# Kernel tuning notes

Measured on AMD Instinct MI355X. Metric: run time of the kernel, lower is better.

Reference implementation:

```python
import jax, jax.numpy as jnp
import numpy as np

DIM = 512
HIDDEN = int(DIM * 0.2)  # 102
K_TOKENS = 64
N_TOKENS = 65536
LN_EPS = 1e-5


def setup_inputs() -> dict:
    key = jax.random.key(0)
    ks = jax.random.split(key, 8)
    x = jax.random.normal(ks[0], (N_TOKENS, DIM), dtype=jnp.float32)
    ln_gamma = jnp.ones((DIM,), dtype=jnp.float32)
    ln_beta = jnp.zeros((DIM,), dtype=jnp.float32)
    W1 = jax.random.normal(ks[1], (DIM, HIDDEN), dtype=jnp.float32) / np.sqrt(DIM)
    b1 = jnp.zeros((HIDDEN,), dtype=jnp.float32)
    W2 = jax.random.normal(ks[2], (HIDDEN, K_TOKENS), dtype=jnp.float32) / np.sqrt(HIDDEN)
    b2 = jnp.zeros((K_TOKENS,), dtype=jnp.float32)
    scale = jnp.ones((1, 1), dtype=jnp.float32)
    return {
        "x": x,
        "ln_gamma": ln_gamma,
        "ln_beta": ln_beta,
        "W1": W1,
        "b1": b1,
        "W2": W2,
        "b2": b2,
        "scale": scale,
        "keeped_tokens": K_TOKENS,
    }


def reference(x, ln_gamma, ln_beta, W1, b1, W2, b2, scale, keeped_tokens):
    # LayerNorm over last dim
    mu = jnp.mean(x, axis=-1, keepdims=True)
    var = jnp.mean(jnp.square(x - mu), axis=-1, keepdims=True)
    h = (x - mu) * jax.lax.rsqrt(var + LN_EPS) * ln_gamma + ln_beta
    # fc1 + exact GELU (torch default) + dynamic fc2 scorer
    h = jax.nn.gelu(h @ W1 + b1, approximate=False)  # [N, HIDDEN]
    w = h @ W2 + b2                                   # [N, K]
    # transpose, scale, softmax over tokens
    w = w.T * scale                                   # [K, N]
    w = jax.nn.softmax(w, axis=1)
    # weighted token aggregation
    return w @ x                                      # [K, DIM]
```

## Files before the change

### kernel.cpp

```cpp
#include <hip/hip_runtime.h>
#include <math.h>

#define N_TOK 65536
#define DIM   512
#define HID   102
#define KTOK  64
#define NTILE 4096
#define LN_EPS 1e-5f

typedef __attribute__((ext_vector_type(8))) short short8;
typedef __attribute__((ext_vector_type(4))) float f32x4;

#define WS_LOGITS 0u
#define WS_PART   4194304u
#define WS_PM     (WS_PART + 4194304u)
#define WS_PS     (WS_PM + 262144u)
#define WS_W1F    (WS_PS + 262144u)
#define WS_W2F    (WS_W1F + 32768u)
#define WS_UB     (WS_W2F + 4096u)
#define WS_VV     (WS_UB + 128u)
#define WS_SMAX   (WS_VV + 128u)
#define WS_SINV   (WS_SMAX + 64u)

__device__ __forceinline__ unsigned short f2bf(float f) {
    unsigned int u = __float_as_uint(f);
    unsigned int r = (u + 0x7fffu + ((u >> 16) & 1u)) >> 16;
    return (unsigned short)r;
}
__device__ __forceinline__ float bf2f(unsigned short h) {
    return __uint_as_float(((unsigned int)h) << 16);
}

__device__ __forceinline__ void gload_lds16(const void* g, void* l) {
    __builtin_amdgcn_global_load_lds(
        (const __attribute__((address_space(1))) unsigned int*)g,
        (__attribute__((address_space(3))) unsigned int*)l, 16, 0, 0);
}

__device__ __forceinline__ void bar_lds() {
    asm volatile("s_waitcnt lgkmcnt(0)" ::: "memory");
    __builtin_amdgcn_s_barrier();
    __builtin_amdgcn_sched_barrier(0);
}

__global__ __launch_bounds__(256) void prep_k(const float* __restrict__ W1,
                                              const float* __restrict__ gamma,
                                              const float* __restrict__ W2,
                                              unsigned short* __restrict__ W1f,
                                              unsigned short* __restrict__ W2f) {
    const int idx = blockIdx.x * 256 + threadIdx.x;
    {
        const int e = idx & 7, lane = (idx >> 3) & 63;
        const int jj = (idx >> 9) & 7, kc = (idx >> 12) & 15;
        const int j = jj * 16 + (lane & 15);
        const int d = kc * 32 + (lane >> 4) * 8 + e;
        W1f[idx] = (j < HID) ? f2bf(gamma[d] * W1[d * HID + j]) : (unsigned short)0;
    }
    if (idx < 8192) {
        const int e = idx & 7, lane = (idx >> 3) & 63;
        const int kc = (idx >> 9) & 3, N = (idx >> 11) & 3;
        const int j = kc * 32 + (lane >> 4) * 8 + e;
        const int k = N * 16 + (lane & 15);
        W2f[idx] = (j < HID) ? f2bf(W2[j * KTOK + k]) : (unsigned short)0;
    }
}

__global__ __launch_bounds__(512) void prep2_k(const float* __restrict__ W1,
                                               const float* __restrict__ b1,
                                               const float* __restrict__ gamma,
                                               const float* __restrict__ beta,
                                               float* __restrict__ ub,
                                               float* __restrict__ vv) {
    __shared__ float su[4][128], sv[4][128];
    const int t = threadIdx.x;
    const int j = t & 127, q = t >> 7;
    float u = 0.0f, v = 0.0f;
    if (j < HID) {
        #pragma unroll 8
        for (int d = q * 128; d < q * 128 + 128; ++d) {
            const float wv = W1[d * HID + j];
            u = fmaf(beta[d], wv, u);
            v = fmaf(gamma[d], wv, v);
        }
    }
    su[q][j] = u; sv[q][j] = v;
    __syncthreads();
    if (q == 0) {
        ub[j] = su[0][j] + su[1][j] + su[2][j] + su[3][j] +
                ((j < HID) ? b1[j] : 0.0f);
        vv[j] = sv[0][j] + sv[1][j] + sv[2][j] + sv[3][j];
    }
}

__global__ __launch_bounds__(512) void scorer_k(const float* __restrict__ x,
                                                const unsigned short* __restrict__ W1f,
                                                const unsigned short* __restrict__ W2f,
                                                const float* __restrict__ ub,
                                                const float* __restrict__ vv,
                                                const float* __restrict__ b2,
                                                const float* __restrict__ scale,
                                                float* __restrict__ logits,
                                                float* __restrict__ pm,
                                                float* __restrict__ psum) {
    __shared__ char smem[4 * 8192];
    const int tid = threadIdx.x;
    const int lane = tid & 63;
    const int w = tid >> 6;
    const int l15 = lane & 15;
    const int hi = lane >> 4;
    const int tile = blockIdx.x * 8 + w;
    const int wt0 = tile * 16;
    char* hb = smem + w * 4096;

    const float* xrow = x + (size_t)(wt0 + l15) * DIM + hi * 8;

    f32x4 xva[5], xvb[5];
    xva[0] = *(const f32x4*)(xrow);
    xvb[0] = *(const f32x4*)(xrow + 4);
    xva[1] = *(const f32x4*)(xrow + 32);
    xvb[1] = *(const f32x4*)(xrow + 36);
    xva[2] = *(const f32x4*)(xrow + 64);
    xvb[2] = *(const f32x4*)(xrow + 68);
    gload_lds16(W1f + w * 512 + lane * 8, smem + w * 1024);
    xva[3] = *(const f32x4*)(xrow + 96);
    xvb[3] = *(const f32x4*)(xrow + 100);
    gload_lds16(W1f + 4096 + w * 512 + lane * 8, smem + 8192 + w * 1024);
    gload_lds16(W1f + 8192 + w * 512 + lane * 8, smem + 16384 + w * 1024);

    f32x4 acc[8] = {};
    float s = 0.0f, ss = 0.0f;
    #pragma unroll
    for (int kc = 0; kc < 16; ++kc) {
        if (kc < 12) {
            xva[(kc + 4) % 5] = *(const f32x4*)(xrow + (kc + 4) * 32);
            xvb[(kc + 4) % 5] = *(const f32x4*)(xrow + (kc + 4) * 32 + 4);
        }
        if (kc <= 1)       asm volatile("s_waitcnt vmcnt(6)" ::: "memory");
        else if (kc <= 11) asm volatile("s_waitcnt vmcnt(8)" ::: "memory");
        else if (kc == 12) asm volatile("s_waitcnt vmcnt(6)" ::: "memory");
        else if (kc == 13) asm volatile("s_waitcnt vmcnt(4)" ::: "memory");
        else if (kc == 14) asm volatile("s_waitcnt vmcnt(1)" ::: "memory");
        else               asm volatile("s_waitcnt vmcnt(0)" ::: "memory");
        __builtin_amdgcn_sched_barrier(0);
        __builtin_amdgcn_s_barrier();
        if (kc < 13) {
            gload_lds16(W1f + (kc + 3) * 4096 + w * 512 + lane * 8,
                        smem + ((kc + 3) & 3) * 8192 + w * 1024);
        }
        const f32x4 a = xva[kc % 5];
        const f32x4 b = xvb[kc % 5];
        s += a.x + a.y + a.z + a.w + b.x + b.y + b.z + b.w;
        ss += a.x * a.x + a.y * a.y + a.z * a.z + a.w * a.w +
              b.x * b.x + b.y * b.y + b.z * b.z + b.w * b.w;
        short8 af;
        af[0] = (short)f2bf(a.x); af[1] = (short)f2bf(a.y);
        af[2] = (short)f2bf(a.z); af[3] = (short)f2bf(a.w);
        af[4] = (short)f2bf(b.x); af[5] = (short)f2bf(b.y);
        af[6] = (short)f2bf(b.z); af[7] = (short)f2bf(b.w);
        const char* bb = smem + (kc & 3) * 8192 + lane * 16;
        __builtin_amdgcn_s_setprio(1);
        #pragma unroll
        for (int jj = 0; jj < 8; ++jj) {
            const short8 bf = *(const short8*)(bb + jj * 1024);
            acc[jj] = __builtin_amdgcn_mfma_f32_16x16x32_bf16(af, bf, acc[jj], 0, 0, 0);
        }
        __builtin_amdgcn_s_setprio(0);
    }
    __syncthreads();

    s += __shfl_xor(s, 16); ss += __shfl_xor(ss, 16);
    s += __shfl_xor(s, 32); ss += __shfl_xor(ss, 32);
    const float mu = s * (1.0f / 512.0f);
    const float inv = rsqrtf(ss * (1.0f / 512.0f) - mu * mu + LN_EPS);

    float invr[4], muir[4];
    #pragma unroll
    for (int r = 0; r < 4; ++r) {
        const int tk = 4 * hi + r;
        const float m_ = __shfl(mu, tk);
        const float i_ = __shfl(inv, tk);
        invr[r] = i_;
        muir[r] = m_ * i_;
    }
    #pragma unroll
    for (int jj = 0; jj < 8; ++jj) {
        const int col = jj * 16 + l15;
        const float ubj = ub[col];
        const float vvj = vv[col];
        #pragma unroll
        for (int reg = 0; reg < 4; ++reg) {
            const int t = 4 * hi + reg;
            const float pre = fmaf(invr[reg], acc[jj][reg],
                                   fmaf(-muir[reg], vvj, ubj));
            const float g = 0.5f * pre * (1.0f + erff(pre * 0.70710678118f));
            *(unsigned short*)(hb + t * 256 + ((col * 2) ^ ((t & 7) << 4))) = f2bf(g);
        }
    }
    asm volatile("s_waitcnt lgkmcnt(0)" ::: "memory");
    __builtin_amdgcn_sched_barrier(0);

    f32x4 acc2[4] = {};
    {
        const unsigned short* w2 = W2f + lane * 8;
        #pragma unroll
        for (int kc = 0; kc < 4; ++kc) {
            const short8 a2 = *(const short8*)(hb + l15 * 256 +
                                               ((kc * 64 + hi * 16) ^ ((l15 & 7) << 4)));
            __builtin_amdgcn_s_setprio(1);
            #pragma unroll
            for (int nt = 0; nt < 4; ++nt) {
                const short8 bfr = *(const short8*)(w2 + (size_t)(nt * 4 + kc) * 512);
                acc2[nt] = __builtin_amdgcn_mfma_f32_16x16x32_bf16(a2, bfr, acc2[nt], 0, 0, 0);
            }
            __builtin_amdgcn_s_setprio(0);
        }
    }

    const float sc = scale[0];
    #pragma unroll
    for (int nt = 0; nt < 4; ++nt) {
        const int k = nt * 16 + l15;
        const float bb = b2[k];
        f32x4 lv;
        lv.x = (acc2[nt][0] + bb) * sc;
        lv.y = (acc2[nt][1] + bb) * sc;
        lv.z = (acc2[nt][2] + bb) * sc;
        lv.w = (acc2[nt][3] + bb) * sc;
        *(f32x4*)(logits + (size_t)k * N_TOK + wt0 + hi * 4) = lv;
        float m4 = fmaxf(fmaxf(lv.x, lv.y), fmaxf(lv.z, lv.w));
        float s4 = __expf(lv.x - m4) + __expf(lv.y - m4) +
                   __expf(lv.z - m4) + __expf(lv.w - m4);
        #pragma unroll
        for (int o = 16; o <= 32; o <<= 1) {
            const float om = __shfl_xor(m4, o);
            const float os = __shfl_xor(s4, o);
            const float nm = fmaxf(m4, om);
            s4 = s4 * __expf(m4 - nm) + os * __expf(om - nm);
            m4 = nm;
        }
        if (hi == 0) {
            pm[tile * 64 + k] = m4;
            psum[tile * 64 + k] = s4;
        }
    }
}

__global__ __launch_bounds__(256) void stats_k(const float* __restrict__ pm,
                                               const float* __restrict__ psum,
                                               float* __restrict__ smax,
                                               float* __restrict__ sinv) {
    const int k = blockIdx.x;
    const int tid = threadIdx.x;
    __shared__ float rm[4], rs[4];
    float m = -1e30f, s = 0.0f;
    for (int b = tid; b < NTILE; b += 256) {
        const float pmv = pm[b * 64 + k];
        const float psv = psum[b * 64 + k];
        const float nm = fmaxf(m, pmv);
        s = s * __expf(m - nm) + psv * __expf(pmv - nm);
        m = nm;
    }
    #pragma unroll
    for (int o = 32; o >= 1; o >>= 1) {
        const float om = __shfl_xor(m, o);
        const float os = __shfl_xor(s, o);
        const float nm = fmaxf(m, om);
        s = s * __expf(m - nm) + os * __expf(om - nm);
        m = nm;
    }
    if ((tid & 63) == 0) { rm[tid >> 6] = m; rs[tid >> 6] = s; }
    __syncthreads();
    if (tid == 0) {
        float fm = rm[0], fs = rs[0];
        for (int i = 1; i < 4; ++i) {
            const float nm = fmaxf(fm, rm[i]);
            fs = fs * __expf(fm - nm) + rs[i] * __expf(rm[i] - nm);
            fm = nm;
        }
        smax[k] = fm;
        sinv[k] = 1.0f / fs;
    }
}

__global__ __launch_bounds__(512) void agg_k(const float* __restrict__ x,
                                             const float* __restrict__ logits,
                                             const float* __restrict__ smax,
                                             const float* __restrict__ sinv,
                                             float* __restrict__ part) {
    __shared__ char fsm[40960];
    const int tid = threadIdx.x;
    const int lane = tid & 63;
    const int w = tid >> 6;
    const int l15 = lane & 15;
    const int hi = lane >> 4;
    const int dg = blockIdx.y;
    const int tb = blockIdx.x;

    const int sk = tid >> 3;
    const int snp = (tid & 7) * 8;
    const int xd = tid & 127;
    const int xnb = (tid >> 7) * 16;
    const float mk = smax[sk];
    const float ik = sinv[sk];
    const float* lrow = logits + (size_t)sk * N_TOK + tb * 512 + snp;
    const float* xcol = x + (size_t)(tb * 512 + xnb) * DIM + dg * 128 + xd;

    char* pw = fsm + (((sk >> 4) * 2 + (snp >> 5)) * 64 +
                      (sk & 15) + 16 * ((snp & 31) >> 3)) * 16;
    const int xoff0 = (((xd >> 4) * 2 + (xnb >> 5)) * 64 +
                       (xd & 15) + 16 * (((xnb & 31) >> 3) + 0)) * 16;
    const int xoff1 = (((xd >> 4) * 2 + (xnb >> 5)) * 64 +
                       (xd & 15) + 16 * (((xnb & 31) >> 3) + 1)) * 16;

    const int kt = w & 3;
    const int dgr = w >> 2;

    f32x4 acc[4] = {};

    f32x4 pa = *(const f32x4*)(lrow);
    f32x4 pb = *(const f32x4*)(lrow + 4);
    float xl[16];
    #pragma unroll
    for (int i = 0; i < 16; ++i) xl[i] = xcol[(size_t)i * DIM];

    for (int c = 0; c < 8; ++c) {
        {
            short8 pv;
            pv[0] = (short)f2bf(__expf(pa.x - mk) * ik);
            pv[1] = (short)f2bf(__expf(pa.y - mk) * ik);
            pv[2] = (short)f2bf(__expf(pa.z - mk) * ik);
            pv[3] = (short)f2bf(__expf(pa.w - mk) * ik);
            pv[4] = (short)f2bf(__expf(pb.x - mk) * ik);
            pv[5] = (short)f2bf(__expf(pb.y - mk) * ik);
            pv[6] = (short)f2bf(__expf(pb.z - mk) * ik);
            pv[7] = (short)f2bf(__expf(pb.w - mk) * ik);
            *(short8*)pw = pv;
        }
        {
            short8 h0, l0, h1, l1;
            #pragma unroll
            for (int e = 0; e < 8; ++e) {
                const float v = xl[e];
                const unsigned short hb16 = f2bf(v);
                h0[e] = (short)hb16;
                l0[e] = (short)f2bf(v - bf2f(hb16));
            }
            #pragma unroll
            for (int e = 0; e < 8; ++e) {
                const float v = xl[8 + e];
                const unsigned short hb16 = f2bf(v);
                h1[e] = (short)hb16;
                l1[e] = (short)f2bf(v - bf2f(hb16));
            }
            *(short8*)(fsm + 8192 + xoff0) = h0;
            *(short8*)(fsm + 24576 + xoff0) = l0;
            *(short8*)(fsm + 8192 + xoff1) = h1;
            *(short8*)(fsm + 24576 + xoff1) = l1;
        }
        f32x4 pa_n, pb_n;
        float xln[16];
        if (c < 7) {
            pa_n = *(const f32x4*)(lrow + (c + 1) * 64);
            pb_n = *(const f32x4*)(lrow + (c + 1) * 64 + 4);
            #pragma unroll
            for (int i = 0; i < 16; ++i)
                xln[i] = xcol[(size_t)((c + 1) * 64 + i) * DIM];
        }
        bar_lds();

        __builtin_amdgcn_s_setprio(1);
        #pragma unroll
        for (int ns = 0; ns < 2; ++ns) {
            const short8 af =
                *(const short8*)(fsm + ((kt * 2 + ns) * 64 + lane) * 16);
            #pragma unroll
            for (int dt = 0; dt < 4; ++dt) {
                const int dti = dgr * 4 + dt;
                const short8 bh = *(const short8*)(fsm + 8192 +
                                                   ((dti * 2 + ns) * 64 + lane) * 16);
                const short8 bl = *(const short8*)(fsm + 24576 +
                                                   ((dti * 2 + ns) * 64 + lane) * 16);
                acc[dt] = __builtin_amdgcn_mfma_f32_16x16x32_bf16(af, bh, acc[dt], 0, 0, 0);
                acc[dt] = __builtin_amdgcn_mfma_f32_16x16x32_bf16(af, bl, acc[dt], 0, 0, 0);
            }
        }
        __builtin_amdgcn_s_setprio(0);
        bar_lds();

        pa = pa_n; pb = pb_n;
        #pragma unroll
        for (int i = 0; i < 16; ++i) xl[i] = xln[i];
    }

    #pragma unroll
    for (int dt = 0; dt < 4; ++dt) {
        const int dcol = dg * 128 + (dgr * 4 + dt) * 16 + l15;
        #pragma unroll
        for (int reg = 0; reg < 4; ++reg) {
            const int k = kt * 16 + 4 * hi + reg;
            part[((size_t)tb * 64 + k) * 512 + dcol] = acc[dt][reg];
        }
    }
}

__global__ __launch_bounds__(256) void reduce_k(const float* __restrict__ part,
                                                float* __restrict__ out) {
    const int idx = blockIdx.x * 256 + threadIdx.x;
    const int k = idx >> 9, d = idx & 511;
    float s = 0.0f;
    for (int tb = 0; tb < 128; ++tb) s += part[((size_t)tb * 64 + k) * 512 + d];
    out[idx] = s;
}

extern "C" void kernel_launch(void* const* d_in, const int* in_sizes, int n_in,
                              void* d_out, int out_size, void* d_ws, size_t ws_size,
                              hipStream_t stream) {
    const float* x     = (const float*)d_in[0];
    const float* gamma = (const float*)d_in[1];
    const float* beta  = (const float*)d_in[2];
    const float* W1    = (const float*)d_in[3];
    const float* b1    = (const float*)d_in[4];
    const float* W2    = (const float*)d_in[5];
    const float* b2    = (const float*)d_in[6];
    const float* scale = (const float*)d_in[7];
    float* out = (float*)d_out;
    float* ws  = (float*)d_ws;

    float* logits = ws + WS_LOGITS;
    float* part   = ws + WS_PART;
    float* pm     = ws + WS_PM;
    float* psum   = ws + WS_PS;
    unsigned short* W1f = (unsigned short*)(ws + WS_W1F);
    unsigned short* W2f = (unsigned short*)(ws + WS_W2F);
    float* ubv  = ws + WS_UB;
    float* vvv  = ws + WS_VV;
    float* smax = ws + WS_SMAX;
    float* sinv = ws + WS_SINV;

    hipLaunchKernelGGL(prep_k, dim3(256), dim3(256), 0, stream,
                       W1, gamma, W2, W1f, W2f);
    hipLaunchKernelGGL(prep2_k, dim3(1), dim3(512), 0, stream,
                       W1, b1, gamma, beta, ubv, vvv);
    hipLaunchKernelGGL(scorer_k, dim3(NTILE / 8), dim3(512), 0, stream,
                       x, W1f, W2f, ubv, vvv, b2, scale, logits, pm, psum);
    hipLaunchKernelGGL(stats_k, dim3(KTOK), dim3(256), 0, stream,
                       pm, psum, smax, sinv);
    hipLaunchKernelGGL(agg_k, dim3(128, 4), dim3(512), 0, stream,
                       x, logits, smax, sinv, part);
    hipLaunchKernelGGL(reduce_k, dim3(128), dim3(256), 0, stream,
                       part, out);
}
```

Before: 108.0 us.

## Restructure scorer fc1 into two column halves with bulk LDS weight staging

The scorer kernel moves to 256-thread blocks of 4 waves. Instead of streaming W1 through a 4-stage ring with a barrier every k-chunk, it loads half of W1's columns (64 KB) into LDS in one shot, then runs all 16 k-chunks with no per-chunk barriers. It does this twice, once per 64-column half. The cost is that each half re-reads the wave's x rows from global memory (twice the x traffic, likely served by cache) and uses 80 KB of LDS per block, which limits occupancy. The aim is to remove the per-iteration barrier syncs and the pipeline bookkeeping.

```diff
diff --git a/kernel.cpp b/kernel.cpp
--- a/kernel.cpp
+++ b/kernel.cpp
@@ -92,7 +92,7 @@
     }
 }
 
-__global__ __launch_bounds__(512) void scorer_k(const float* __restrict__ x,
+__global__ __launch_bounds__(256) void scorer_k(const float* __restrict__ x,
                                                 const unsigned short* __restrict__ W1f,
                                                 const unsigned short* __restrict__ W2f,
                                                 const float* __restrict__ ub,
@@ -102,98 +102,106 @@
                                                 float* __restrict__ logits,
                                                 float* __restrict__ pm,
                                                 float* __restrict__ psum) {
-    __shared__ char smem[4 * 8192];
+    __shared__ char smem[65536 + 16384];
     const int tid = threadIdx.x;
     const int lane = tid & 63;
     const int w = tid >> 6;
     const int l15 = lane & 15;
     const int hi = lane >> 4;
-    const int tile = blockIdx.x * 8 + w;
+    const int tile = blockIdx.x * 4 + w;
     const int wt0 = tile * 16;
-    char* hb = smem + w * 4096;
+    char* hb = smem + 65536 + w * 4096;
 
     const float* xrow = x + (size_t)(wt0 + l15) * DIM + hi * 8;
-
-    f32x4 xva[5], xvb[5];
-    xva[0] = *(const f32x4*)(xrow);
-    xvb[0] = *(const f32x4*)(xrow + 4);
-    xva[1] = *(const f32x4*)(xrow + 32);
-    xvb[1] = *(const f32x4*)(xrow + 36);
-    xva[2] = *(const f32x4*)(xrow + 64);
-    xvb[2] = *(const f32x4*)(xrow + 68);
-    gload_lds16(W1f + w * 512 + lane * 8, smem + w * 1024);
-    xva[3] = *(const f32x4*)(xrow + 96);
-    xvb[3] = *(const f32x4*)(xrow + 100);
-    gload_lds16(W1f + 4096 + w * 512 + lane * 8, smem + 8192 + w * 1024);
-    gload_lds16(W1f + 8192 + w * 512 + lane * 8, smem + 16384 + w * 1024);
 
     f32x4 acc[8] = {};
     float s = 0.0f, ss = 0.0f;
+    float mu = 0.0f, inv = 0.0f;
+
     #pragma unroll
-    for (int kc = 0; kc < 16; ++kc) {
-        if (kc < 12) {
-            xva[(kc + 4) % 5] = *(const f32x4*)(xrow + (kc + 4) * 32);
-            xvb[(kc + 4) % 5] = *(const f32x4*)(xrow + (kc + 4) * 32 + 4);
-        }
-        if (kc <= 1)       asm volatile("s_waitcnt vmcnt(6)" ::: "memory");
-        else if (kc <= 11) asm volatile("s_waitcnt vmcnt(8)" ::: "memory");
-        else if (kc == 12) asm volatile("s_waitcnt vmcnt(6)" ::: "memory");
-        else if (kc == 13) asm volatile("s_waitcnt vmcnt(4)" ::: "memory");
-        else if (kc == 14) asm volatile("s_waitcnt vmcnt(1)" ::: "memory");
-        else               asm volatile("s_waitcnt vmcnt(0)" ::: "memory");
+    for (int half = 0; half < 2; ++half) {
+        if (half == 1) bar_lds();
+        #pragma unroll
+        for (int r = 0; r < 4; ++r) {
+            const int kc = w * 4 + r;
+            #pragma unroll
+            for (int j = 0; j < 4; ++j)
+                gload_lds16(W1f + kc * 4096 + (half * 4 + j) * 512 + lane * 8,
+                            smem + kc * 4096 + j * 1024 + lane * 16);
+        }
+        f32x4 xva[5], xvb[5];
+        #pragma unroll
+        for (int g = 0; g < 4; ++g) {
+            xva[g] = *(const f32x4*)(xrow + g * 32);
+            xvb[g] = *(const f32x4*)(xrow + g * 32 + 4);
+        }
+        asm volatile("s_waitcnt vmcnt(8)" ::: "memory");
         __builtin_amdgcn_sched_barrier(0);
         __builtin_amdgcn_s_barrier();
-        if (kc < 13) {
-            gload_lds16(W1f + (kc + 3) * 4096 + w * 512 + lane * 8,
-                        smem + ((kc + 3) & 3) * 8192 + w * 1024);
-        }
-        const f32x4 a = xva[kc % 5];
-        const f32x4 b = xvb[kc % 5];
-        s += a.x + a.y + a.z + a.w + b.x + b.y + b.z + b.w;
-        ss += a.x * a.x + a.y * a.y + a.z * a.z + a.w * a.w +
-              b.x * b.x + b.y * b.y + b.z * b.z + b.w * b.w;
-        short8 af;
-        af[0] = (short)f2bf(a.x); af[1] = (short)f2bf(a.y);
-        af[2] = (short)f2bf(a.z); af[3] = (short)f2bf(a.w);
-        af[4] = (short)f2bf(b.x); af[5] = (short)f2bf(b.y);
-        af[6] = (short)f2bf(b.z); af[7] = (short)f2bf(b.w);
-        const char* bb = smem + (kc & 3) * 8192 + lane * 16;
-        __builtin_amdgcn_s_setprio(1);
-        #pragma unroll
-        for (int jj = 0; jj < 8; ++jj) {
-            const short8 bf = *(const short8*)(bb + jj * 1024);
-            acc[jj] = __builtin_amdgcn_mfma_f32_16x16x32_bf16(af, bf, acc[jj], 0, 0, 0);
-        }
-        __builtin_amdgcn_s_setprio(0);
-    }
-    __syncthreads();
-
-    s += __shfl_xor(s, 16); ss += __shfl_xor(ss, 16);
-    s += __shfl_xor(s, 32); ss += __shfl_xor(ss, 32);
-    const float mu = s * (1.0f / 512.0f);
-    const float inv = rsqrtf(ss * (1.0f / 512.0f) - mu * mu + LN_EPS);
-
-    float invr[4], muir[4];
-    #pragma unroll
-    for (int r = 0; r < 4; ++r) {
-        const int tk = 4 * hi + r;
-        const float m_ = __shfl(mu, tk);
-        const float i_ = __shfl(inv, tk);
-        invr[r] = i_;
-        muir[r] = m_ * i_;
-    }
-    #pragma unroll
-    for (int jj = 0; jj < 8; ++jj) {
-        const int col = jj * 16 + l15;
-        const float ubj = ub[col];
-        const float vvj = vv[col];
-        #pragma unroll
-        for (int reg = 0; reg < 4; ++reg) {
-            const int t = 4 * hi + reg;
-            const float pre = fmaf(invr[reg], acc[jj][reg],
-                                   fmaf(-muir[reg], vvj, ubj));
-            const float g = 0.5f * pre * (1.0f + erff(pre * 0.70710678118f));
-            *(unsigned short*)(hb + t * 256 + ((col * 2) ^ ((t & 7) << 4))) = f2bf(g);
+        #pragma unroll
+        for (int kc = 0; kc < 16; ++kc) {
+            if (kc <= 11) {
+                xva[(kc + 4) % 5] = *(const f32x4*)(xrow + (kc + 4) * 32);
+                xvb[(kc + 4) % 5] = *(const f32x4*)(xrow + (kc + 4) * 32 + 4);
+            }
+            if (kc <= 11)      asm volatile("s_waitcnt vmcnt(8)" ::: "memory");
+            else if (kc == 12) asm volatile("s_waitcnt vmcnt(6)" ::: "memory");
+            else if (kc == 13) asm volatile("s_waitcnt vmcnt(4)" ::: "memory");
+            else if (kc == 14) asm volatile("s_waitcnt vmcnt(2)" ::: "memory");
+            else               asm volatile("s_waitcnt vmcnt(0)" ::: "memory");
+            __builtin_amdgcn_sched_barrier(0);
+            const f32x4 a = xva[kc % 5];
+            const f32x4 b = xvb[kc % 5];
+            if (half == 0) {
+                s += a.x + a.y + a.z + a.w + b.x + b.y + b.z + b.w;
+                ss += a.x * a.x + a.y * a.y + a.z * a.z + a.w * a.w +
+                      b.x * b.x + b.y * b.y + b.z * b.z + b.w * b.w;
+            }
+            short8 af;
+            af[0] = (short)f2bf(a.x); af[1] = (short)f2bf(a.y);
+            af[2] = (short)f2bf(a.z); af[3] = (short)f2bf(a.w);
+            af[4] = (short)f2bf(b.x); af[5] = (short)f2bf(b.y);
+            af[6] = (short)f2bf(b.z); af[7] = (short)f2bf(b.w);
+            const char* bb = smem + kc * 4096 + lane * 16;
+            __builtin_amdgcn_s_setprio(1);
+            #pragma unroll
+            for (int j = 0; j < 4; ++j) {
+                const short8 bf = *(const short8*)(bb + j * 1024);
+                acc[half * 4 + j] =
+                    __builtin_amdgcn_mfma_f32_16x16x32_bf16(af, bf, acc[half * 4 + j], 0, 0, 0);
+            }
+            __builtin_amdgcn_s_setprio(0);
+        }
+
+        if (half == 0) {
+            s += __shfl_xor(s, 16); ss += __shfl_xor(ss, 16);
+            s += __shfl_xor(s, 32); ss += __shfl_xor(ss, 32);
+            mu = s * (1.0f / 512.0f);
+            inv = rsqrtf(ss * (1.0f / 512.0f) - mu * mu + LN_EPS);
+        }
+
+        float invr[4], muir[4];
+        #pragma unroll
+        for (int r = 0; r < 4; ++r) {
+            const int tk = 4 * hi + r;
+            const float m_ = __shfl(mu, tk);
+            const float i_ = __shfl(inv, tk);
+            invr[r] = i_;
+            muir[r] = m_ * i_;
+        }
+        #pragma unroll
+        for (int j = 0; j < 4; ++j) {
+            const int col = half * 64 + j * 16 + l15;
+            const float ubj = ub[col];
+            const float vvj = vv[col];
+            #pragma unroll
+            for (int reg = 0; reg < 4; ++reg) {
+                const int t = 4 * hi + reg;
+                const float pre = fmaf(invr[reg], acc[half * 4 + j][reg],
+                                       fmaf(-muir[reg], vvj, ubj));
+                const float g = 0.5f * pre * (1.0f + erff(pre * 0.70710678118f));
+                *(unsigned short*)(hb + t * 256 + ((col * 2) ^ ((t & 7) << 4))) = f2bf(g);
+            }
         }
     }
     asm volatile("s_waitcnt lgkmcnt(0)" ::: "memory");
@@ -441,7 +449,7 @@
                        W1, gamma, W2, W1f, W2f);
     hipLaunchKernelGGL(prep2_k, dim3(1), dim3(512), 0, stream,
                        W1, b1, gamma, beta, ubv, vvv);
-    hipLaunchKernelGGL(scorer_k, dim3(NTILE / 8), dim3(512), 0, stream,
+    hipLaunchKernelGGL(scorer_k, dim3(NTILE / 4), dim3(256), 0, stream,
                        x, W1f, W2f, ubv, vvv, b2, scale, logits, pm, psum);
     hipLaunchKernelGGL(stats_k, dim3(KTOK), dim3(256), 0, stream,
                        pm, psum, smax, sinv);
```

After: 120.1 us. 11.2% more time.
